# Kernel tuning notes

Measured on AMD Instinct MI355X. Metric: run time of the kernel, lower is better.

The kernel has to match this reference:

```python
import jax, jax.numpy as jnp
import numpy as np

N_NODES = 10000
N_EDGES = 160000
D = 512            # input_dim = hidden_size = output_dim
NUM_EXPERTS = 4
N_LAYERS = 2


def setup_inputs() -> dict:
    key = jax.random.key(0)
    k = jax.random.split(key, 7)
    x = jax.random.normal(k[0], (N_NODES, D), dtype=jnp.float32)
    edge_index = jax.random.randint(k[1], (2, N_EDGES), 0, N_NODES, dtype=jnp.int32)
    # Gating network (Linear D -> NUM_EXPERTS)
    gate_w = jax.random.normal(k[2], (D, NUM_EXPERTS), dtype=jnp.float32) * 0.05
    gate_b = jnp.zeros((NUM_EXPERTS,), dtype=jnp.float32)
    # Per-expert SAGEConv weights: lin_r (self/root) and lin_l (neighbor) + bias
    w_self = jax.random.normal(k[3], (NUM_EXPERTS, N_LAYERS, D, D), dtype=jnp.float32) * 0.05
    w_neigh = jax.random.normal(k[4], (NUM_EXPERTS, N_LAYERS, D, D), dtype=jnp.float32) * 0.05
    b_exp = jnp.zeros((NUM_EXPERTS, N_LAYERS, D), dtype=jnp.float32)
    return {"x": x, "edge_index": edge_index, "gate_w": gate_w, "gate_b": gate_b,
            "w_self": w_self, "w_neigh": w_neigh, "b_exp": b_exp, "top_k": 1}


def reference(x, edge_index, gate_w, gate_b, w_self, w_neigh, b_exp, top_k):
    n = x.shape[0]
    src, dst = edge_index[0], edge_index[1]
    # mean-aggregation normalization (PyG SAGEConv aggr='mean'); 0 for isolated nodes
    deg = jax.ops.segment_sum(jnp.ones_like(src, dtype=x.dtype), dst, num_segments=n)
    inv_deg = jnp.where(deg > 0, 1.0 / jnp.maximum(deg, 1.0), 0.0)[:, None]  # [N,1]

    # gating: softmax(Linear(x)) then top-k routing
    gate = jax.nn.softmax(x @ gate_w + gate_b, axis=-1)          # [N, E]
    top_vals, top_idx = jax.lax.top_k(gate, top_k)               # [N, k]

    def expert(ws, wn, b):  # ws, wn: [L, D, D]; b: [L, D]
        h = x
        for l in range(N_LAYERS):
            agg = jax.ops.segment_sum(h[src], dst, num_segments=n) * inv_deg
            # SAGEConv: lin_l(mean_neigh) + lin_r(x) + bias, then relu (norm='id', eval dropout)
            h = jax.nn.relu(agg @ wn[l] + h @ ws[l] + b[l])
        return h

    # dense all-expert compute (matches original module)
    outs = jax.vmap(expert)(w_self, w_neigh, b_exp)              # [E, N, D]
    outs = jnp.transpose(outs, (1, 0, 2))                        # [N, E, D]
    sel = jnp.take_along_axis(outs, top_idx[:, :, None], axis=1)  # [N, k, D]
    return jnp.sum(sel * top_vals[:, :, None], axis=1)           # [N, D]
```

## Files before the change

### kernel.cpp

```cpp
#include <hip/hip_runtime.h>
#include <hip/hip_bf16.h>
#include <cstdint>

#define N_NODES 10000
#define N_EDGES 160000
#define DIM 512
#define K1 1024
#define NEXP 4

typedef __bf16 bf16_t;
typedef bf16_t bf16x8 __attribute__((ext_vector_type(8)));
typedef float f32x4 __attribute__((ext_vector_type(4)));

#define AS1(p) ((__attribute__((address_space(1))) void*)(p))
#define AS3(p) ((__attribute__((address_space(3))) void*)(p))

__global__ void zero_kernel(int* __restrict__ deg, int* __restrict__ ecnt) {
    int i = blockIdx.x * blockDim.x + threadIdx.x;
    if (i < N_NODES) deg[i] = 0;
    if (i < NEXP) ecnt[i] = 0;
}

__global__ void gate_kernel(const float* __restrict__ x,
                            const float* __restrict__ gw,
                            const float* __restrict__ gb,
                            int* __restrict__ top_idx,
                            float* __restrict__ top_val,
                            bf16_t* __restrict__ acat) {
    const int wave = threadIdx.x >> 6;
    const int lane = threadIdx.x & 63;
    const int node = blockIdx.x * 4 + wave;
    if (node >= N_NODES) return;
    const float4* x4 = (const float4*)(x + (size_t)node * DIM);
    const float4* gw4 = (const float4*)gw;
    float4 xa = x4[lane * 2];
    float4 xb = x4[lane * 2 + 1];
    float xv[8] = { xa.x, xa.y, xa.z, xa.w, xb.x, xb.y, xb.z, xb.w };
    float a0 = 0.f, a1 = 0.f, a2 = 0.f, a3 = 0.f;
    #pragma unroll
    for (int c = 0; c < 8; c++) {
        float4 g = gw4[lane * 8 + c];
        a0 += xv[c] * g.x; a1 += xv[c] * g.y; a2 += xv[c] * g.z; a3 += xv[c] * g.w;
    }
    bf16x8 o;
    #pragma unroll
    for (int c = 0; c < 8; c++) o[c] = (bf16_t)xv[c];
    *(bf16x8*)(acat + (size_t)node * K1 + DIM + lane * 8) = o;
    for (int off = 32; off > 0; off >>= 1) {
        a0 += __shfl_xor(a0, off);
        a1 += __shfl_xor(a1, off);
        a2 += __shfl_xor(a2, off);
        a3 += __shfl_xor(a3, off);
    }
    if (lane == 0) {
        float z[4] = { a0 + gb[0], a1 + gb[1], a2 + gb[2], a3 + gb[3] };
        int bi = 0; float bm = z[0];
        for (int e = 1; e < 4; e++) if (z[e] > bm) { bm = z[e]; bi = e; }
        float den = 0.f;
        for (int e = 0; e < 4; e++) den += expf(z[e] - bm);
        top_idx[node] = bi;
        top_val[node] = 1.0f / den;
    }
}

__global__ void bucket_kernel(const int* __restrict__ top_idx,
                              int* __restrict__ ecnt,
                              int* __restrict__ lists) {
    __shared__ int lcnt[NEXP];
    __shared__ int base[NEXP];
    const int tid = threadIdx.x;
    if (tid < NEXP) lcnt[tid] = 0;
    __syncthreads();
    const int node = blockIdx.x * 256 + tid;
    int e = 0, rank = 0;
    if (node < N_NODES) {
        e = top_idx[node];
        rank = atomicAdd(&lcnt[e], 1);
    }
    __syncthreads();
    if (tid < NEXP) base[tid] = atomicAdd(&ecnt[tid], lcnt[tid]);
    __syncthreads();
    if (node < N_NODES) lists[e * N_NODES + base[e] + rank] = node;
}

__global__ void deg_kernel(const int* __restrict__ dst, int* __restrict__ deg) {
    int i = blockIdx.x * blockDim.x + threadIdx.x;
    if (i < N_EDGES) atomicAdd(&deg[dst[i]], 1);
}

__global__ void scan_kernel(const int* __restrict__ deg,
                            int* __restrict__ offs,
                            int* __restrict__ cursor) {
    __shared__ int wsum[16];
    __shared__ int carrysh;
    const int tid = threadIdx.x;
    const int lane = tid & 63;
    const int wv = tid >> 6;
    if (tid == 0) carrysh = 0;
    __syncthreads();
    for (int base = 0; base < N_NODES; base += 1024) {
        int i = base + tid;
        int v = (i < N_NODES) ? deg[i] : 0;
        int s = v;
        #pragma unroll
        for (int off = 1; off < 64; off <<= 1) {
            int t = __shfl_up(s, off);
            if (lane >= off) s += t;
        }
        if (lane == 63) wsum[wv] = s;
        int carry = carrysh;
        __syncthreads();
        if (wv == 0) {
            int w = (lane < 16) ? wsum[lane] : 0;
            #pragma unroll
            for (int off = 1; off < 16; off <<= 1) {
                int t = __shfl_up(w, off);
                if (lane >= off) w += t;
            }
            if (lane < 16) wsum[lane] = w;
        }
        __syncthreads();
        int wbase = (wv > 0) ? wsum[wv - 1] : 0;
        int excl = carry + wbase + s - v;
        if (i < N_NODES) { offs[i] = excl; cursor[i] = excl; }
        int total = wsum[15];
        __syncthreads();
        if (tid == 0) carrysh = carry + total;
        __syncthreads();
    }
    if (tid == 0) offs[N_NODES] = carrysh;
}

__global__ void fill_kernel(const int* __restrict__ src, const int* __restrict__ dst,
                            int* __restrict__ cursor, int* __restrict__ csr) {
    int i = blockIdx.x * blockDim.x + threadIdx.x;
    if (i < N_EDGES) {
        int d = dst[i];
        int p = atomicAdd(&cursor[d], 1);
        csr[p] = src[i];
    }
}

__global__ void wtrans_kernel(const float* __restrict__ w_neigh,
                              const float* __restrict__ w_self,
                              bf16_t* __restrict__ Bt) {
    __shared__ float tile[32][33];
    const int m = blockIdx.z;
    const bool isSelf = m >= 8;
    const int el = m & 7;
    const float* W = (isSelf ? w_self : w_neigh) + (size_t)el * DIM * DIM;
    const int k0 = blockIdx.x * 32;
    const int n0 = blockIdx.y * 32;
    const int tx = threadIdx.x, ty = threadIdx.y;
    for (int r = ty; r < 32; r += 8)
        tile[r][tx] = W[(size_t)(k0 + r) * DIM + n0 + tx];
    __syncthreads();
    for (int r = ty; r < 32; r += 8) {
        int n = n0 + r;
        int k = k0 + tx;
        Bt[((size_t)el * DIM + n) * K1 + (isSelf ? DIM : 0) + k] = (bf16_t)tile[tx][r];
    }
}

__global__ void agg1_kernel(const int* __restrict__ offs, const int* __restrict__ csr,
                            const int* __restrict__ deg, bf16_t* __restrict__ acat) {
    const int wave = threadIdx.x >> 6;
    const int lane = threadIdx.x & 63;
    const int node = blockIdx.x * 4 + wave;
    if (node >= N_NODES) return;
    const int c0 = lane * 8;
    float s[8] = {0,0,0,0,0,0,0,0};
    int beg = offs[node];
    int d = deg[node];
    int end = beg + d;
    int p = beg;
    for (; p + 1 < end; p += 2) {
        int s0 = csr[p], s1 = csr[p + 1];
        bf16x8 v0 = *(const bf16x8*)(acat + (size_t)s0 * K1 + DIM + c0);
        bf16x8 v1 = *(const bf16x8*)(acat + (size_t)s1 * K1 + DIM + c0);
        #pragma unroll
        for (int k = 0; k < 8; k++) s[k] += (float)v0[k] + (float)v1[k];
    }
    if (p < end) {
        int s0 = csr[p];
        bf16x8 v0 = *(const bf16x8*)(acat + (size_t)s0 * K1 + DIM + c0);
        #pragma unroll
        for (int k = 0; k < 8; k++) s[k] += (float)v0[k];
    }
    float w = d > 0 ? 1.0f / (float)d : 0.0f;
    bf16x8 o;
    #pragma unroll
    for (int k = 0; k < 8; k++) o[k] = (bf16_t)(s[k] * w);
    *(bf16x8*)(acat + (size_t)node * K1 + c0) = o;
}

__global__ void agg2_kernel(const int* __restrict__ offs, const int* __restrict__ csr,
                            const int* __restrict__ deg, const int* __restrict__ top_idx,
                            const bf16_t* __restrict__ h1, bf16_t* __restrict__ acat) {
    const int wave = threadIdx.x >> 6;
    const int lane = threadIdx.x & 63;
    const int node = blockIdx.x * 4 + wave;
    if (node >= N_NODES) return;
    const int c0 = lane * 8;
    const bf16_t* hb = h1 + (size_t)top_idx[node] * N_NODES * DIM;
    float s[8] = {0,0,0,0,0,0,0,0};
    int beg = offs[node];
    int d = deg[node];
    int end = beg + d;
    int p = beg;
    for (; p + 1 < end; p += 2) {
        int s0 = csr[p], s1 = csr[p + 1];
        bf16x8 v0 = *(const bf16x8*)(hb + (size_t)s0 * DIM + c0);
        bf16x8 v1 = *(const bf16x8*)(hb + (size_t)s1 * DIM + c0);
        #pragma unroll
        for (int k = 0; k < 8; k++) s[k] += (float)v0[k] + (float)v1[k];
    }
    if (p < end) {
        int s0 = csr[p];
        bf16x8 v0 = *(const bf16x8*)(hb + (size_t)s0 * DIM + c0);
        #pragma unroll
        for (int k = 0; k < 8; k++) s[k] += (float)v0[k];
    }
    float w = d > 0 ? 1.0f / (float)d : 0.0f;
    bf16x8 o;
    #pragma unroll
    for (int k = 0; k < 8; k++) o[k] = (bf16_t)(s[k] * w);
    *(bf16x8*)(acat + (size_t)node * K1 + c0) = o;
    *(bf16x8*)(acat + (size_t)node * K1 + DIM + c0) = *(const bf16x8*)(hb + (size_t)node * DIM + c0);
}

template <int MODE>
__global__ __launch_bounds__(256)
void gemm_kernel(const bf16_t* __restrict__ A,
                 const bf16_t* __restrict__ Bt,
                 const int layer,
                 const float* __restrict__ bias_all,
                 bf16_t* __restrict__ h1,
                 float* __restrict__ out,
                 const int* __restrict__ lists,
                 const int* __restrict__ ecnt,
                 const float* __restrict__ top_val) {
    const int e = blockIdx.z;
    int cnt = N_NODES;
    if (MODE == 1) {
        cnt = ecnt[e];
        if ((int)(blockIdx.y * 128) >= cnt) return;
    }
    __shared__ __align__(16) bf16_t As[128 * 32];
    __shared__ __align__(16) bf16_t Bs[128 * 32];

    const int t = threadIdx.x;
    const int lane = t & 63;
    const int wave = t >> 6;
    const int wm = wave >> 1;
    const int wn = wave & 1;

    const int r0 = t >> 2;
    const int kc = (t & 3) * 8;

    int i0 = blockIdx.y * 128 + r0;
    int i1 = i0 + 64;
    int arow0, arow1;
    if (MODE == 0) {
        arow0 = min(i0, N_NODES - 1);
        arow1 = min(i1, N_NODES - 1);
    } else {
        arow0 = lists[e * N_NODES + min(i0, cnt - 1)];
        arow1 = lists[e * N_NODES + min(i1, cnt - 1)];
    }
    const bf16_t* aptr0 = A + (size_t)arow0 * K1 + kc;
    const bf16_t* aptr1 = A + (size_t)arow1 * K1 + kc;
    const bf16_t* Bte = Bt + (size_t)(e * 2 + layer) * DIM * K1;
    const bf16_t* bptr0 = Bte + (size_t)(blockIdx.x * 128 + r0) * K1 + kc;
    const bf16_t* bptr1 = bptr0 + (size_t)64 * K1;

    f32x4 acc[4][4] = {};

    char* asb = (char*)&As[0];
    char* bsb = (char*)&Bs[0];
    const int wb = wave * 1024;

    for (int k0 = 0; k0 < K1; k0 += 32) {
        __syncthreads();
        __builtin_amdgcn_global_load_lds(AS1(aptr0), AS3(asb + wb),        16, 0, 0);
        __builtin_amdgcn_global_load_lds(AS1(aptr1), AS3(asb + 4096 + wb), 16, 0, 0);
        __builtin_amdgcn_global_load_lds(AS1(bptr0), AS3(bsb + wb),        16, 0, 0);
        __builtin_amdgcn_global_load_lds(AS1(bptr1), AS3(bsb + 4096 + wb), 16, 0, 0);
        __syncthreads();
        bf16x8 af[4], bfr[4];
        #pragma unroll
        for (int i = 0; i < 4; i++)
            af[i] = *(const bf16x8*)(As + (wm * 64 + i * 16 + (lane & 15)) * 32 + (lane >> 4) * 8);
        #pragma unroll
        for (int j = 0; j < 4; j++)
            bfr[j] = *(const bf16x8*)(Bs + (wn * 64 + j * 16 + (lane & 15)) * 32 + (lane >> 4) * 8);
        #pragma unroll
        for (int i = 0; i < 4; i++)
            #pragma unroll
            for (int j = 0; j < 4; j++)
                acc[i][j] = __builtin_amdgcn_mfma_f32_16x16x32_bf16(af[i], bfr[j], acc[i][j], 0, 0, 0);
        aptr0 += 32; aptr1 += 32; bptr0 += 32; bptr1 += 32;
    }

    const float* bias = bias_all + e * 1024 + layer * DIM;
    const int cbase = blockIdx.x * 128 + wn * 64 + (lane & 15);
    float bv[4];
    #pragma unroll
    for (int j = 0; j < 4; j++) bv[j] = bias[cbase + j * 16];
    #pragma unroll
    for (int i = 0; i < 4; i++) {
        #pragma unroll
        for (int r = 0; r < 4; r++) {
            int row = blockIdx.y * 128 + wm * 64 + i * 16 + (lane >> 4) * 4 + r;
            if (MODE == 0) {
                if (row < N_NODES) {
                    bf16_t* cp = h1 + ((size_t)e * N_NODES + row) * DIM + cbase;
                    #pragma unroll
                    for (int j = 0; j < 4; j++) {
                        float v = fmaxf(acc[i][j][r] + bv[j], 0.f);
                        cp[j * 16] = (bf16_t)v;
                    }
                }
            } else {
                if (row < cnt) {
                    int node = lists[e * N_NODES + row];
                    float tv = top_val[node];
                    float* cp = out + (size_t)node * DIM + cbase;
                    #pragma unroll
                    for (int j = 0; j < 4; j++) {
                        float v = fmaxf(acc[i][j][r] + bv[j], 0.f);
                        cp[j * 16] = v * tv;
                    }
                }
            }
        }
    }
}

extern "C" void kernel_launch(void* const* d_in, const int* in_sizes, int n_in,
                              void* d_out, int out_size, void* d_ws, size_t ws_size,
                              hipStream_t stream) {
    const float* x       = (const float*)d_in[0];
    const int*   edge    = (const int*)d_in[1];
    const float* gw      = (const float*)d_in[2];
    const float* gb      = (const float*)d_in[3];
    const float* w_self  = (const float*)d_in[4];
    const float* w_neigh = (const float*)d_in[5];
    const float* b_exp   = (const float*)d_in[6];
    float* out = (float*)d_out;

    char* p = (char*)d_ws;
    auto alloc = [&](size_t bytes) {
        char* r = p;
        p += (bytes + 255) & ~(size_t)255;
        return r;
    };
    bf16_t* Bt      = (bf16_t*)alloc((size_t)8 * DIM * K1 * 2);
    bf16_t* acat    = (bf16_t*)alloc((size_t)N_NODES * K1 * 2);
    bf16_t* h1      = (bf16_t*)alloc((size_t)NEXP * N_NODES * DIM * 2);
    int*    deg     = (int*)alloc((size_t)N_NODES * 4);
    int*    offs    = (int*)alloc((size_t)(N_NODES + 1) * 4);
    int*    cursor  = (int*)alloc((size_t)N_NODES * 4);
    int*    csr     = (int*)alloc((size_t)N_EDGES * 4);
    int*    top_idx = (int*)alloc((size_t)N_NODES * 4);
    float*  top_val = (float*)alloc((size_t)N_NODES * 4);
    int*    ecnt    = (int*)alloc(256);
    int*    lists   = (int*)alloc((size_t)NEXP * N_NODES * 4);

    const int* srcE = edge;
    const int* dstE = edge + N_EDGES;

    zero_kernel<<<40, 256, 0, stream>>>(deg, ecnt);
    gate_kernel<<<N_NODES / 4, 256, 0, stream>>>(x, gw, gb, top_idx, top_val, acat);
    bucket_kernel<<<40, 256, 0, stream>>>(top_idx, ecnt, lists);
    deg_kernel<<<N_EDGES / 256, 256, 0, stream>>>(dstE, deg);
    scan_kernel<<<1, 1024, 0, stream>>>(deg, offs, cursor);
    fill_kernel<<<N_EDGES / 256, 256, 0, stream>>>(srcE, dstE, cursor, csr);
    wtrans_kernel<<<dim3(16, 16, 16), dim3(32, 8), 0, stream>>>(w_neigh, w_self, Bt);
    agg1_kernel<<<N_NODES / 4, 256, 0, stream>>>(offs, csr, deg, acat);
    gemm_kernel<0><<<dim3(4, 79, 4), 256, 0, stream>>>(acat, Bt, 0, b_exp, h1, nullptr, nullptr, nullptr, nullptr);
    agg2_kernel<<<N_NODES / 4, 256, 0, stream>>>(offs, csr, deg, top_idx, h1, acat);
    gemm_kernel<1><<<dim3(4, 79, 4), 256, 0, stream>>>(acat, Bt, 1, b_exp, nullptr, out, lists, ecnt, top_val);
}
```

Baseline: 298.0 us.

## Double GEMM K-tile to 64 with new LDS layout; unroll aggregation gathers by 4

Result: slower. 328.9 us (+10.4%).

```diff
diff --git a/kernel.cpp b/kernel.cpp
--- a/kernel.cpp
+++ b/kernel.cpp
@@ -163,7 +163,7 @@
 }
 
 __global__ void agg1_kernel(const int* __restrict__ offs, const int* __restrict__ csr,
-                            const int* __restrict__ deg, bf16_t* __restrict__ acat) {
+                            bf16_t* __restrict__ acat) {
     const int wave = threadIdx.x >> 6;
     const int lane = threadIdx.x & 63;
     const int node = blockIdx.x * 4 + wave;
@@ -171,19 +171,22 @@
     const int c0 = lane * 8;
     float s[8] = {0,0,0,0,0,0,0,0};
     int beg = offs[node];
-    int d = deg[node];
-    int end = beg + d;
+    int end = offs[node + 1];
+    int d = end - beg;
     int p = beg;
-    for (; p + 1 < end; p += 2) {
-        int s0 = csr[p], s1 = csr[p + 1];
-        bf16x8 v0 = *(const bf16x8*)(acat + (size_t)s0 * K1 + DIM + c0);
-        bf16x8 v1 = *(const bf16x8*)(acat + (size_t)s1 * K1 + DIM + c0);
-        #pragma unroll
-        for (int k = 0; k < 8; k++) s[k] += (float)v0[k] + (float)v1[k];
-    }
-    if (p < end) {
-        int s0 = csr[p];
-        bf16x8 v0 = *(const bf16x8*)(acat + (size_t)s0 * K1 + DIM + c0);
+    for (; p + 4 <= end; p += 4) {
+        int i0 = csr[p], i1 = csr[p + 1], i2 = csr[p + 2], i3 = csr[p + 3];
+        bf16x8 v0 = *(const bf16x8*)(acat + (size_t)i0 * K1 + DIM + c0);
+        bf16x8 v1 = *(const bf16x8*)(acat + (size_t)i1 * K1 + DIM + c0);
+        bf16x8 v2 = *(const bf16x8*)(acat + (size_t)i2 * K1 + DIM + c0);
+        bf16x8 v3 = *(const bf16x8*)(acat + (size_t)i3 * K1 + DIM + c0);
+        #pragma unroll
+        for (int k = 0; k < 8; k++)
+            s[k] += ((float)v0[k] + (float)v1[k]) + ((float)v2[k] + (float)v3[k]);
+    }
+    for (; p < end; p++) {
+        int i0 = csr[p];
+        bf16x8 v0 = *(const bf16x8*)(acat + (size_t)i0 * K1 + DIM + c0);
         #pragma unroll
         for (int k = 0; k < 8; k++) s[k] += (float)v0[k];
     }
@@ -195,7 +198,7 @@
 }
 
 __global__ void agg2_kernel(const int* __restrict__ offs, const int* __restrict__ csr,
-                            const int* __restrict__ deg, const int* __restrict__ top_idx,
+                            const int* __restrict__ top_idx,
                             const bf16_t* __restrict__ h1, bf16_t* __restrict__ acat) {
     const int wave = threadIdx.x >> 6;
     const int lane = threadIdx.x & 63;
@@ -205,19 +208,22 @@
     const bf16_t* hb = h1 + (size_t)top_idx[node] * N_NODES * DIM;
     float s[8] = {0,0,0,0,0,0,0,0};
     int beg = offs[node];
-    int d = deg[node];
-    int end = beg + d;
+    int end = offs[node + 1];
+    int d = end - beg;
     int p = beg;
-    for (; p + 1 < end; p += 2) {
-        int s0 = csr[p], s1 = csr[p + 1];
-        bf16x8 v0 = *(const bf16x8*)(hb + (size_t)s0 * DIM + c0);
-        bf16x8 v1 = *(const bf16x8*)(hb + (size_t)s1 * DIM + c0);
-        #pragma unroll
-        for (int k = 0; k < 8; k++) s[k] += (float)v0[k] + (float)v1[k];
-    }
-    if (p < end) {
-        int s0 = csr[p];
-        bf16x8 v0 = *(const bf16x8*)(hb + (size_t)s0 * DIM + c0);
+    for (; p + 4 <= end; p += 4) {
+        int i0 = csr[p], i1 = csr[p + 1], i2 = csr[p + 2], i3 = csr[p + 3];
+        bf16x8 v0 = *(const bf16x8*)(hb + (size_t)i0 * DIM + c0);
+        bf16x8 v1 = *(const bf16x8*)(hb + (size_t)i1 * DIM + c0);
+        bf16x8 v2 = *(const bf16x8*)(hb + (size_t)i2 * DIM + c0);
+        bf16x8 v3 = *(const bf16x8*)(hb + (size_t)i3 * DIM + c0);
+        #pragma unroll
+        for (int k = 0; k < 8; k++)
+            s[k] += ((float)v0[k] + (float)v1[k]) + ((float)v2[k] + (float)v3[k]);
+    }
+    for (; p < end; p++) {
+        int i0 = csr[p];
+        bf16x8 v0 = *(const bf16x8*)(hb + (size_t)i0 * DIM + c0);
         #pragma unroll
         for (int k = 0; k < 8; k++) s[k] += (float)v0[k];
     }
@@ -246,60 +252,64 @@
         cnt = ecnt[e];
         if ((int)(blockIdx.y * 128) >= cnt) return;
     }
-    __shared__ __align__(16) bf16_t As[128 * 32];
-    __shared__ __align__(16) bf16_t Bs[128 * 32];
+    __shared__ __align__(16) bf16_t As[128 * 64];
+    __shared__ __align__(16) bf16_t Bs[128 * 64];
 
     const int t = threadIdx.x;
     const int lane = t & 63;
     const int wave = t >> 6;
     const int wm = wave >> 1;
     const int wn = wave & 1;
-
-    const int r0 = t >> 2;
-    const int kc = (t & 3) * 8;
-
-    int i0 = blockIdx.y * 128 + r0;
-    int i1 = i0 + 64;
-    int arow0, arow1;
-    if (MODE == 0) {
-        arow0 = min(i0, N_NODES - 1);
-        arow1 = min(i1, N_NODES - 1);
-    } else {
-        arow0 = lists[e * N_NODES + min(i0, cnt - 1)];
-        arow1 = lists[e * N_NODES + min(i1, cnt - 1)];
-    }
-    const bf16_t* aptr0 = A + (size_t)arow0 * K1 + kc;
-    const bf16_t* aptr1 = A + (size_t)arow1 * K1 + kc;
+    const int wa = wave >> 1;
+    const int wh = wave & 1;
+    const int lr = t & 15;
+    const int lc = (t >> 4) & 3;
+
     const bf16_t* Bte = Bt + (size_t)(e * 2 + layer) * DIM * K1;
-    const bf16_t* bptr0 = Bte + (size_t)(blockIdx.x * 128 + r0) * K1 + kc;
-    const bf16_t* bptr1 = bptr0 + (size_t)64 * K1;
+    const bf16_t* aptr[4];
+    const bf16_t* bptr[4];
+    #pragma unroll
+    for (int j = 0; j < 4; j++) {
+        int rb = 2 * j + wa;
+        int i0 = blockIdx.y * 128 + rb * 16 + lr;
+        int arow;
+        if (MODE == 0) arow = min(i0, N_NODES - 1);
+        else           arow = lists[e * N_NODES + min(i0, cnt - 1)];
+        aptr[j] = A + (size_t)arow * K1 + wh * 32 + lc * 8;
+        int brow = blockIdx.x * 128 + rb * 16 + lr;
+        bptr[j] = Bte + (size_t)brow * K1 + wh * 32 + lc * 8;
+    }
 
     f32x4 acc[4][4] = {};
-
     char* asb = (char*)&As[0];
     char* bsb = (char*)&Bs[0];
-    const int wb = wave * 1024;
-
-    for (int k0 = 0; k0 < K1; k0 += 32) {
-        __syncthreads();
-        __builtin_amdgcn_global_load_lds(AS1(aptr0), AS3(asb + wb),        16, 0, 0);
-        __builtin_amdgcn_global_load_lds(AS1(aptr1), AS3(asb + 4096 + wb), 16, 0, 0);
-        __builtin_amdgcn_global_load_lds(AS1(bptr0), AS3(bsb + wb),        16, 0, 0);
-        __builtin_amdgcn_global_load_lds(AS1(bptr1), AS3(bsb + 4096 + wb), 16, 0, 0);
-        __syncthreads();
-        bf16x8 af[4], bfr[4];
-        #pragma unroll
-        for (int i = 0; i < 4; i++)
-            af[i] = *(const bf16x8*)(As + (wm * 64 + i * 16 + (lane & 15)) * 32 + (lane >> 4) * 8);
+
+    for (int k0 = 0; k0 < K1; k0 += 64) {
+        __syncthreads();
         #pragma unroll
         for (int j = 0; j < 4; j++)
-            bfr[j] = *(const bf16x8*)(Bs + (wn * 64 + j * 16 + (lane & 15)) * 32 + (lane >> 4) * 8);
-        #pragma unroll
-        for (int i = 0; i < 4; i++)
+            __builtin_amdgcn_global_load_lds(AS1(aptr[j]), AS3(asb + (4 * j + wave) * 1024), 16, 0, 0);
+        #pragma unroll
+        for (int j = 0; j < 4; j++)
+            __builtin_amdgcn_global_load_lds(AS1(bptr[j]), AS3(bsb + (4 * j + wave) * 1024), 16, 0, 0);
+        __syncthreads();
+        #pragma unroll
+        for (int h = 0; h < 2; h++) {
+            bf16x8 af[4], bfr[4];
+            #pragma unroll
+            for (int i = 0; i < 4; i++)
+                af[i] = *(const bf16x8*)(As + (8 * wm + 2 * i + h) * 512 + (lane >> 4) * 128 + (lane & 15) * 8);
             #pragma unroll
             for (int j = 0; j < 4; j++)
-                acc[i][j] = __builtin_amdgcn_mfma_f32_16x16x32_bf16(af[i], bfr[j], acc[i][j], 0, 0, 0);
-        aptr0 += 32; aptr1 += 32; bptr0 += 32; bptr1 += 32;
+                bfr[j] = *(const bf16x8*)(Bs + (8 * wn + 2 * j + h) * 512 + (lane >> 4) * 128 + (lane & 15) * 8);
+            #pragma unroll
+            for (int i = 0; i < 4; i++)
+                #pragma unroll
+                for (int j = 0; j < 4; j++)
+                    acc[i][j] = __builtin_amdgcn_mfma_f32_16x16x32_bf16(af[i], bfr[j], acc[i][j], 0, 0, 0);
+        }
+        #pragma unroll
+        for (int j = 0; j < 4; j++) { aptr[j] += 64; bptr[j] += 64; }
     }
 
     const float* bias = bias_all + e * 1024 + layer * DIM;
@@ -377,8 +387,8 @@
     scan_kernel<<<1, 1024, 0, stream>>>(deg, offs, cursor);
     fill_kernel<<<N_EDGES / 256, 256, 0, stream>>>(srcE, dstE, cursor, csr);
     wtrans_kernel<<<dim3(16, 16, 16), dim3(32, 8), 0, stream>>>(w_neigh, w_self, Bt);
-    agg1_kernel<<<N_NODES / 4, 256, 0, stream>>>(offs, csr, deg, acat);
+    agg1_kernel<<<N_NODES / 4, 256, 0, stream>>>(offs, csr, acat);
     gemm_kernel<0><<<dim3(4, 79, 4), 256, 0, stream>>>(acat, Bt, 0, b_exp, h1, nullptr, nullptr, nullptr, nullptr);
-    agg2_kernel<<<N_NODES / 4, 256, 0, stream>>>(offs, csr, deg, top_idx, h1, acat);
+    agg2_kernel<<<N_NODES / 4, 256, 0, stream>>>(offs, csr, top_idx, h1, acat);
     gemm_kernel<1><<<dim3(4, 79, 4), 256, 0, stream>>>(acat, Bt, 1, b_exp, nullptr, out, lists, ecnt, top_val);
 }
```
